# Kernel tuning notes

Hardware: AMD Instinct MI355X
Metric: run time of the kernel (lower is better)

## Reference

```python
import jax, jax.numpy as jnp
import numpy as np

B, S, H, NH = 2, 2048, 768, 12
HD = H // NH
MEM_W = 0.5  # memory_weight
LN_EPS = 1e-5


def setup_inputs() -> dict:
    key = jax.random.key(0)
    ks = jax.random.split(key, 12)
    xav = lambda k: jax.random.uniform(k, (H, H), jnp.float32, -1.0, 1.0) * np.sqrt(6.0 / (H + H))
    return {
        "hidden_states": jax.random.normal(ks[0], (B, S, H), jnp.float32),
        "cross_states": jax.random.normal(ks[1], (B, S, H), jnp.float32),
        "attention_mask": jnp.ones((B, 1, S, S), jnp.int32),
        "memory_tensors": jax.random.normal(ks[2], (2, B, S, H), jnp.float32),
        "dynamic_factor": jax.random.uniform(ks[3], (B, S, 1), jnp.float32),
        "Wq": xav(ks[4]), "bq": jnp.zeros((H,), jnp.float32),
        "Wk": xav(ks[5]), "bk": jnp.zeros((H,), jnp.float32),
        "Wv": xav(ks[6]), "bv": jnp.zeros((H,), jnp.float32),
        "Wo": xav(ks[7]), "bo": jnp.zeros((H,), jnp.float32),
        "gate": jnp.ones((1,), jnp.float32),
        "gate_bias": jnp.zeros((1,), jnp.float32),
        "ln_g": jnp.ones((H,), jnp.float32),
        "ln_b": jnp.zeros((H,), jnp.float32),
    }


def _layernorm(x, g, b):
    mu = jnp.mean(x, axis=-1, keepdims=True)
    var = jnp.mean(jnp.square(x - mu), axis=-1, keepdims=True)
    return (x - mu) * jax.lax.rsqrt(var + LN_EPS) * g + b


def reference(hidden_states, cross_states, attention_mask, memory_tensors,
              dynamic_factor, Wq, bq, Wk, bk, Wv, bv, Wo, bo,
              gate, gate_bias, ln_g, ln_b):
    x = _layernorm(hidden_states, ln_g, ln_b)
    q = x @ Wq + bq                      # [B,S,H]
    k = cross_states @ Wk + bk
    v = cross_states @ Wv + bv
    k = k + memory_tensors[0] * MEM_W    # memory injection into K/V
    v = v + memory_tensors[1] * MEM_W

    q = q.reshape(B, S, NH, HD).transpose(0, 2, 1, 3)  # [B,NH,S,HD]
    k = k.reshape(B, S, NH, HD).transpose(0, 2, 1, 3)
    v = v.reshape(B, S, NH, HD).transpose(0, 2, 1, 3)

    scores = jnp.einsum("bhqd,bhkd->bhqk", q, k) / np.sqrt(HD)
    scores = jnp.where(attention_mask == 0, -jnp.inf, scores)
    attn = jax.nn.softmax(scores, axis=-1)
    out = jnp.einsum("bhqk,bhkd->bhqd", attn, v)       # [B,NH,S,HD]
    out = out.transpose(0, 2, 1, 3).reshape(B, S, H)

    out = out @ Wo + bo
    out = out * gate + gate_bias
    out = out * dynamic_factor
    return out
```

## Files before the change

### kernel.cpp

```cpp
#include <hip/hip_runtime.h>
#include <hip/hip_bf16.h>
#include <stdint.h>

#define BB   2
#define SS   2048
#define HH   768
#define NHH  12
#define HDD  64
#define BSS  (BB*SS)
#define NBH  (BB*NHH)
#define ROWS_BH (NBH*SS)
#define NSPLIT 2

typedef unsigned short u16;
typedef unsigned int   u32;
typedef __attribute__((ext_vector_type(8))) short bf16x8_t;
typedef __attribute__((ext_vector_type(4))) float f32x4;
typedef __attribute__((ext_vector_type(2))) u32   u32x2;
typedef __attribute__((ext_vector_type(4))) u32   u32x4;

#define MFMA16(a, b, c) __builtin_amdgcn_mfma_f32_16x16x32_bf16((a), (b), (c), 0, 0, 0)

__device__ __forceinline__ float b2f(u16 u) {
    u32 x = ((u32)u) << 16; float f; __builtin_memcpy(&f, &x, 4); return f;
}
__device__ __forceinline__ u16 f2b(float f) {
    u32 x; __builtin_memcpy(&x, &f, 4);
    u32 r = x + 0x7fffu + ((x >> 16) & 1u);
    return (u16)(r >> 16);
}
__device__ __forceinline__ void async16(const u16* g, u16* l) {
    __builtin_amdgcn_global_load_lds(
        (const __attribute__((address_space(1))) void*)g,
        (__attribute__((address_space(3))) void*)l, 16, 0, 0);
}

__global__ __launch_bounds__(256) void prep_kernel(
    const float* __restrict__ Wq, const float* __restrict__ Wk,
    const float* __restrict__ Wv, const float* __restrict__ Wo,
    u16* __restrict__ Wt,
    const float* __restrict__ hid, const float* __restrict__ cross,
    const float* __restrict__ g, const float* __restrict__ bb,
    u16* __restrict__ xln, u16* __restrict__ crossb,
    const int* __restrict__ mask, u32* __restrict__ bits,
    u32* __restrict__ wrow)
{
    int id = blockIdx.x;
    int t = threadIdx.x;

    if (id < 576) {
        int mat = id / 144, rem = id % 144;
        int by = rem / 12, bx = rem % 12;
        const float* src = (mat == 0) ? Wq : (mat == 1) ? Wk : (mat == 2) ? Wv : Wo;
        u16* dst = Wt + (size_t)mat * 768 * 768;

        __shared__ float sm[64][68];
        int r0 = by * 64, c0 = bx * 64;
        #pragma unroll
        for (int it = 0; it < 4; ++it) {
            int c = t + it * 256;
            int r = c >> 4, sg = c & 15;
            *(float4*)&sm[r][sg * 4] = *(const float4*)&src[(size_t)(r0 + r) * 768 + c0 + sg * 4];
        }
        __syncthreads();
        #pragma unroll
        for (int it = 0; it < 2; ++it) {
            int c = t + it * 256;
            int rr = c >> 3, sg = c & 7;
            u16 tmp[8] __attribute__((aligned(16)));
            #pragma unroll
            for (int j = 0; j < 8; ++j) tmp[j] = f2b(sm[sg * 8 + j][rr]);
            *(u32x4*)&dst[(size_t)(c0 + rr) * 768 + r0 + sg * 8] = *(u32x4*)tmp;
        }
        return;
    }

    if (id < 2624) {
        int lid = id - 576;
        int y = lid >> 10, bx = lid & 1023;
        int wv = t >> 6, lane = t & 63;
        int row = bx * 4 + wv;

        if (y == 1) {
            const float* xr = cross + (size_t)row * 768;
            u16* o = crossb + (size_t)row * 768;
            #pragma unroll
            for (int c = 0; c < 3; ++c) {
                float4 f = *(const float4*)&xr[c * 256 + lane * 4];
                u16 t4[4] __attribute__((aligned(8)));
                t4[0] = f2b(f.x); t4[1] = f2b(f.y); t4[2] = f2b(f.z); t4[3] = f2b(f.w);
                *(u32x2*)&o[c * 256 + lane * 4] = *(u32x2*)t4;
            }
            return;
        }

        const float* xr = hid + (size_t)row * 768;
        float v[12];
        float s = 0.f, s2 = 0.f;
        #pragma unroll
        for (int c = 0; c < 3; ++c) {
            float4 f = *(const float4*)&xr[c * 256 + lane * 4];
            v[c*4+0] = f.x; v[c*4+1] = f.y; v[c*4+2] = f.z; v[c*4+3] = f.w;
            s  += f.x + f.y + f.z + f.w;
            s2 += f.x*f.x + f.y*f.y + f.z*f.z + f.w*f.w;
        }
        #pragma unroll
        for (int off = 1; off < 64; off <<= 1) {
            s  += __shfl_xor(s,  off, 64);
            s2 += __shfl_xor(s2, off, 64);
        }
        float mu  = s  * (1.f / 768.f);
        float var = s2 * (1.f / 768.f) - mu * mu;
        float rs  = 1.f / sqrtf(var + 1e-5f);
        #pragma unroll
        for (int c = 0; c < 3; ++c) {
            float4 gg = *(const float4*)&g [c * 256 + lane * 4];
            float4 bv = *(const float4*)&bb[c * 256 + lane * 4];
            u16 o[4] __attribute__((aligned(8)));
            o[0] = f2b((v[c*4+0] - mu) * rs * gg.x + bv.x);
            o[1] = f2b((v[c*4+1] - mu) * rs * gg.y + bv.y);
            o[2] = f2b((v[c*4+2] - mu) * rs * gg.z + bv.z);
            o[3] = f2b((v[c*4+3] - mu) * rs * gg.w + bv.w);
            *(u32x2*)&xln[(size_t)row * 768 + c * 256 + lane * 4] = *(u32x2*)o;
        }
        return;
    }

    {
        int mid = id - 2624;
        int w = mid * 256 + t;
        const int4* p = (const int4*)(mask + (size_t)w * 32);
        u32 v = 0;
        #pragma unroll
        for (int i = 0; i < 8; ++i) {
            int4 m = p[i];
            v |= ((m.x != 0) ? 1u : 0u) << (4 * i + 0);
            v |= ((m.y != 0) ? 1u : 0u) << (4 * i + 1);
            v |= ((m.z != 0) ? 1u : 0u) << (4 * i + 2);
            v |= ((m.w != 0) ? 1u : 0u) << (4 * i + 3);
        }
        bits[w] = v;
        unsigned long long ball = __ballot(v == 0xffffffffu);
        if ((t & 63) == 0) {
            u32 wr = 0;
            #pragma unroll
            for (int kt = 0; kt < 32; ++kt)
                if (((ball >> (2 * kt)) & 3ull) == 3ull) wr |= (1u << kt);
            wrow[w >> 6] = wr;
        }
    }
}

__device__ __forceinline__ void gemm128_main(const u16* __restrict__ A,
                                             const u16* __restrict__ W,
                                             f32x4 acc[4][4])
{
    __shared__ __attribute__((aligned(16))) u16 AsL[128 * 64];
    __shared__ __attribute__((aligned(16))) u16 BsL[128 * 64];
    int m0 = blockIdx.x * 128, n0 = blockIdx.y * 128;
    int t = threadIdx.x;
    int wv = t >> 6, lane = t & 63, lm = lane & 15, quad = lane >> 4;
    int wr = wv >> 1, wc = wv & 1;

    for (int kt = 0; kt < 768 / 64; ++kt) {
        __syncthreads();
        #pragma unroll
        for (int it = 0; it < 4; ++it) {
            int c = t + it * 256;
            int row = c >> 3, cs = (c & 7) ^ (row & 7);
            async16(A + (size_t)(m0 + row) * 768 + kt * 64 + cs * 8, &AsL[c * 8]);
            async16(W + (size_t)(n0 + row) * 768 + kt * 64 + cs * 8, &BsL[c * 8]);
        }
        __syncthreads();
        #pragma unroll
        for (int kk = 0; kk < 2; ++kk) {
            bf16x8_t af[4], bfv[4];
            #pragma unroll
            for (int i = 0; i < 4; ++i) {
                int r = wr * 64 + i * 16 + lm;
                af[i] = *(const bf16x8_t*)&AsL[(r * 8 + ((kk * 4 + quad) ^ (r & 7))) * 8];
            }
            #pragma unroll
            for (int j = 0; j < 4; ++j) {
                int r = wc * 64 + j * 16 + lm;
                bfv[j] = *(const bf16x8_t*)&BsL[(r * 8 + ((kk * 4 + quad) ^ (r & 7))) * 8];
            }
            #pragma unroll
            for (int i = 0; i < 4; ++i)
                #pragma unroll
                for (int j = 0; j < 4; ++j)
                    acc[i][j] = MFMA16(af[i], bfv[j], acc[i][j]);
        }
    }
}

__global__ __launch_bounds__(256) void qkv_gemm(
    const u16* __restrict__ xln, const u16* __restrict__ crossb,
    const u16* __restrict__ Wt,  const float* __restrict__ bq,
    const float* __restrict__ bk, const float* __restrict__ bv,
    const float* __restrict__ mem,
    u16* __restrict__ Qb, u16* __restrict__ Kb, u16* __restrict__ VtG)
{
    int z = blockIdx.z;
    const u16* A      = (z == 0) ? xln : crossb;
    const u16* W      = Wt + (size_t)z * 768 * 768;
    const float* bias = (z == 0) ? bq : (z == 1) ? bk : bv;
    const float* mp   = (z == 0) ? (const float*)nullptr : mem + (size_t)(z - 1) * BSS * HH;

    f32x4 z4 = {0.f, 0.f, 0.f, 0.f};
    f32x4 acc[4][4];
    #pragma unroll
    for (int i = 0; i < 4; ++i)
        #pragma unroll
        for (int j = 0; j < 4; ++j) acc[i][j] = z4;

    gemm128_main(A, W, acc);

    int t = threadIdx.x, wv = t >> 6, lane = t & 63, lm = lane & 15, quad = lane >> 4;
    int wr = wv >> 1, wc = wv & 1;
    int row0 = blockIdx.x * 128 + wr * 64 + quad * 4;
    int col0 = blockIdx.y * 128 + wc * 64 + lm;

    if (z == 2) {
        #pragma unroll
        for (int j = 0; j < 4; ++j) {
            int cg = col0 + j * 16;
            float bz = bias[cg];
            int h = cg >> 6, d = cg & 63;
            #pragma unroll
            for (int i = 0; i < 4; ++i) {
                int rg = row0 + i * 16;
                int b = rg >> 11, s = rg & 2047;
                u16 ob[4] __attribute__((aligned(8)));
                #pragma unroll
                for (int e = 0; e < 4; ++e) {
                    float v = acc[i][j][e] + bz + 0.5f * mp[(size_t)(rg + e) * HH + cg];
                    ob[e] = f2b(v);
                }
                *(u32x2*)&VtG[((size_t)(b * NHH + h) * 64 + d) * SS + s] = *(u32x2*)ob;
            }
        }
        return;
    }

    u16* out = (z == 0) ? Qb : Kb;
    #pragma unroll
    for (int j = 0; j < 4; ++j) {
        int cg = col0 + j * 16;
        float bz = bias[cg];
        #pragma unroll
        for (int i = 0; i < 4; ++i) {
            int rg = row0 + i * 16;
            #pragma unroll
            for (int e = 0; e < 4; ++e) {
                float v = acc[i][j][e] + bz;
                if (mp) v += 0.5f * mp[(size_t)(rg + e) * HH + cg];
                out[(size_t)(rg + e) * HH + cg] = f2b(v);
            }
        }
    }
}

__global__ __launch_bounds__(512) void attn_kernel(
    const u16* __restrict__ Q, const u16* __restrict__ K,
    const u16* __restrict__ VtG, const u32* __restrict__ mbits,
    const u32* __restrict__ wrow,
    u16* __restrict__ Pacc, float* __restrict__ Pl, int ksteps)
{
    __shared__ __attribute__((aligned(16))) u16   KsL[64 * 64];
    __shared__ __attribute__((aligned(16))) u16   VtL[64 * 64];
    __shared__ __attribute__((aligned(16))) short Ps[8][16][72];

    int qt = blockIdx.x;
    int bh = blockIdx.y;
    int z  = blockIdx.z;
    int b = bh / NHH, h = bh % NHH;
    int t = threadIdx.x;
    int wv = t >> 6, lane = t & 63, lm = lane & 15, quad = lane >> 4;
    int r7 = lm & 7;

    int qrow_g = b * SS + qt * 128 + wv * 16;
    const u16* qp = Q + (size_t)(qrow_g + lm) * HH + h * 64;
    bf16x8_t qf0 = *(const bf16x8_t*)&qp[quad * 8];
    bf16x8_t qf1 = *(const bf16x8_t*)&qp[32 + quad * 8];

    f32x4 z4 = {0.f, 0.f, 0.f, 0.f};
    f32x4 acc_o[4] = {z4, z4, z4, z4};
    float l_part[4] = {0.f, 0.f, 0.f, 0.f};

    const float SC = 0.18033688011112042f;
    int qloc = qt * 128 + wv * 16 + quad * 4;

    u32 wand = wrow[b * SS + qloc + 0] & wrow[b * SS + qloc + 1] &
               wrow[b * SS + qloc + 2] & wrow[b * SS + qloc + 3];

    int kr = t >> 3, cs = (t & 7) ^ (kr & 7);
    const u16* Kb0 = K + (size_t)(b * SS) * HH + h * 64;
    const u16* Vb0 = VtG + (size_t)bh * 64 * SS;

    int kt0 = z * ksteps;
    for (int kt = kt0; kt < kt0 + ksteps; ++kt) {
        __syncthreads();
        int k0 = kt * 64;
        async16(Kb0 + (size_t)(k0 + kr) * HH + cs * 8, &KsL[t * 8]);
        async16(Vb0 + (size_t)kr * SS + k0 + cs * 8,   &VtL[t * 8]);
        __syncthreads();

        f32x4 sc[4];
        #pragma unroll
        for (int k16 = 0; k16 < 4; ++k16) {
            int rowk = k16 * 16 + lm;
            bf16x8_t kf0 = *(const bf16x8_t*)&KsL[(rowk * 8 + (quad ^ r7)) * 8];
            bf16x8_t kf1 = *(const bf16x8_t*)&KsL[(rowk * 8 + ((quad ^ 4) ^ r7)) * 8];
            f32x4 a = z4;
            a = MFMA16(qf0, kf0, a);
            a = MFMA16(qf1, kf1, a);
            sc[k16] = a;
        }

        if (!__all((int)((wand >> kt) & 1u))) {
            #pragma unroll
            for (int e = 0; e < 4; ++e) {
                u32x2 u = *(const u32x2*)&mbits[(size_t)(b * SS + qloc + e) * (SS / 32) + kt * 2];
                unsigned long long mw = ((unsigned long long)u.y << 32) | (unsigned long long)u.x;
                #pragma unroll
                for (int k16 = 0; k16 < 4; ++k16)
                    if (!((mw >> (k16 * 16 + lm)) & 1ull)) sc[k16][e] = -3.0e38f;
            }
        }

        #pragma unroll
        for (int k16 = 0; k16 < 4; ++k16) {
            #pragma unroll
            for (int e = 0; e < 4; ++e) {
                float p = __builtin_amdgcn_exp2f(sc[k16][e] * SC);
                sc[k16][e] = p;
                l_part[e] += p;
            }
        }

        #pragma unroll
        for (int k16 = 0; k16 < 4; ++k16) {
            int colg = ((k16 + quad) & 3) * 16;
            #pragma unroll
            for (int e = 0; e < 4; ++e) {
                float pv = sc[k16][e];
                u32 pb = __builtin_bit_cast(u32, pv);
                Ps[wv][quad * 4 + e][colg + lm] = (short)((pb + 0x8000u) >> 16);
            }
        }
        __asm__ volatile("" ::: "memory");

        #pragma unroll
        for (int cc = 0; cc < 2; ++cc) {
            int k16r = cc * 2 + (quad >> 1);
            int colg = ((k16r + (lm >> 2)) & 3) * 16 + (quad & 1) * 8;
            bf16x8_t pf = *(const bf16x8_t*)&Ps[wv][lm][colg];
            #pragma unroll
            for (int j = 0; j < 4; ++j) {
                bf16x8_t vf = *(const bf16x8_t*)&VtL[((j * 16 + lm) * 8 + ((cc * 4 + quad) ^ r7)) * 8];
                acc_o[j] = MFMA16(pf, vf, acc_o[j]);
            }
        }
    }

    #pragma unroll
    for (int off = 1; off < 16; off <<= 1) {
        #pragma unroll
        for (int e = 0; e < 4; ++e)
            l_part[e] += __shfl_xor(l_part[e], off, 64);
    }

    size_t prow = ((size_t)z * NBH + bh) * SS + qt * 128 + wv * 16 + quad * 4;
    #pragma unroll
    for (int j = 0; j < 4; ++j)
        #pragma unroll
        for (int e = 0; e < 4; ++e)
            Pacc[(prow + e) * 64 + j * 16 + lm] = f2b(acc_o[j][e]);
    if (lm == 0) {
        #pragma unroll
        for (int e = 0; e < 4; ++e)
            Pl[prow + e] = l_part[e];
    }
}

__global__ __launch_bounds__(256) void attn_merge(
    const u16* __restrict__ Pacc, const float* __restrict__ Pl,
    u16* __restrict__ AO)
{
    int t = threadIdx.x;
    int r = blockIdx.x * 64 + (t >> 2);
    int dseg = (t & 3) * 16;

    float lsum = Pl[r] + Pl[(size_t)ROWS_BH + r];

    float o[16];
    #pragma unroll
    for (int i = 0; i < 16; ++i) o[i] = 0.f;
    #pragma unroll
    for (int s = 0; s < NSPLIT; ++s) {
        const u16* ap = &Pacc[((size_t)s * ROWS_BH + r) * 64 + dseg];
        u32x4 a0 = *(const u32x4*)ap;
        u32x4 a1 = *(const u32x4*)(ap + 8);
        u32 wa[8];
        wa[0]=a0.x; wa[1]=a0.y; wa[2]=a0.z; wa[3]=a0.w;
        wa[4]=a1.x; wa[5]=a1.y; wa[6]=a1.z; wa[7]=a1.w;
        #pragma unroll
        for (int i = 0; i < 8; ++i) {
            o[2*i]   += b2f((u16)(wa[i] & 0xffff));
            o[2*i+1] += b2f((u16)(wa[i] >> 16));
        }
    }
    float inv = 1.f / lsum;
    int bh = r >> 11, q = r & 2047;
    int b = bh / NHH, h = bh % NHH;
    u16 ob[16] __attribute__((aligned(16)));
    #pragma unroll
    for (int i = 0; i < 16; ++i) ob[i] = f2b(o[i] * inv);
    u16* op = &AO[((size_t)(b * SS + q)) * HH + h * 64 + dseg];
    *(u32x4*)op       = *(u32x4*)ob;
    *(u32x4*)(op + 8) = *(u32x4*)(ob + 8);
}

__global__ __launch_bounds__(256) void out_gemm(
    const u16* __restrict__ AO, const u16* __restrict__ Wt,
    const float* __restrict__ bo, const float* __restrict__ gate,
    const float* __restrict__ gbias, const float* __restrict__ dyn,
    float* __restrict__ out)
{
    f32x4 z4 = {0.f, 0.f, 0.f, 0.f};
    f32x4 acc[4][4];
    #pragma unroll
    for (int i = 0; i < 4; ++i)
        #pragma unroll
        for (int j = 0; j < 4; ++j) acc[i][j] = z4;

    gemm128_main(AO, Wt, acc);

    float gv = gate[0];
    float gb = gbias[0];
    int t = threadIdx.x, wv = t >> 6, lane = t & 63, lm = lane & 15, quad = lane >> 4;
    int wr = wv >> 1, wc = wv & 1;
    int row0 = blockIdx.x * 128 + wr * 64 + quad * 4;
    int col0 = blockIdx.y * 128 + wc * 64 + lm;
    #pragma unroll
    for (int j = 0; j < 4; ++j) {
        int cg = col0 + j * 16;
        float bz = bo[cg];
        #pragma unroll
        for (int i = 0; i < 4; ++i) {
            int rg = row0 + i * 16;
            #pragma unroll
            for (int e = 0; e < 4; ++e) {
                float v = acc[i][j][e] + bz;
                v = v * gv + gb;
                v *= dyn[rg + e];
                out[(size_t)(rg + e) * HH + cg] = v;
            }
        }
    }
}

extern "C" void kernel_launch(void* const* d_in, const int* in_sizes, int n_in,
                              void* d_out, int out_size, void* d_ws, size_t ws_size,
                              hipStream_t stream)
{
    (void)in_sizes; (void)n_in; (void)out_size; (void)ws_size;

    const float* hid   = (const float*)d_in[0];
    const float* cross = (const float*)d_in[1];
    const int*   amask = (const int*)d_in[2];
    const float* mem   = (const float*)d_in[3];
    const float* dyn   = (const float*)d_in[4];
    const float* Wq    = (const float*)d_in[5];
    const float* bq    = (const float*)d_in[6];
    const float* Wk    = (const float*)d_in[7];
    const float* bk    = (const float*)d_in[8];
    const float* Wv    = (const float*)d_in[9];
    const float* bv    = (const float*)d_in[10];
    const float* Wo    = (const float*)d_in[11];
    const float* bo    = (const float*)d_in[12];
    const float* gate  = (const float*)d_in[13];
    const float* gbias = (const float*)d_in[14];
    const float* lng   = (const float*)d_in[15];
    const float* lnb   = (const float*)d_in[16];

    char* p = (char*)d_ws;
    u16* Wt   = (u16*)p; p += (size_t)4 * 768 * 768 * 2;
    u32* mb   = (u32*)p; p += (size_t)BB * SS * (SS / 32) * 4;
    u32* wrow = (u32*)p; p += (size_t)BSS * 4;
    u16* xln  = (u16*)p; p += (size_t)BSS * HH * 2;
    u16* crb  = (u16*)p; p += (size_t)BSS * HH * 2;
    u16* Qb   = (u16*)p; p += (size_t)BSS * HH * 2;
    u16* Kb   = (u16*)p; p += (size_t)BSS * HH * 2;
    u16* VtG  = (u16*)p; p += (size_t)BSS * HH * 2;
    u16* Pacc  = xln;
    float* Pl  = (float*)Wt;
    u16* AO    = Kb;

    prep_kernel <<<dim3(3648),           256, 0, stream>>>(
        Wq, Wk, Wv, Wo, Wt, hid, cross, lng, lnb, xln, crb, amask, mb, wrow);
    qkv_gemm    <<<dim3(32, 6, 3),       256, 0, stream>>>(
        xln, crb, Wt, bq, bk, bv, mem, Qb, Kb, VtG);
    attn_kernel <<<dim3(16, 24, NSPLIT), 512, 0, stream>>>(
        Qb, Kb, VtG, mb, wrow, Pacc, Pl, SS / 64 / NSPLIT);
    attn_merge  <<<dim3(ROWS_BH / 64),   256, 0, stream>>>(Pacc, Pl, AO);
    out_gemm    <<<dim3(32, 6),          256, 0, stream>>>(
        AO, Wt + (size_t)3 * 768 * 768, bo, gate, gbias, dyn, (float*)d_out);
}
```

Measured before the change: 262.2 us.

## Double-buffer LDS tiles in GEMMs and attention, move GEMMs to 8 waves

The attention kernel and the shared GEMM mainloop now use double-buffered LDS tiles. The next K/V or A/W tile is prefetched asynchronously while the current one is consumed, and only one barrier is needed per iteration. This is meant to hide global-load latency behind MFMA work. The GEMMs also move from 256 to 512 threads with a 4x2 MFMA tile per wave and a K-step of 32, and they drop the XOR swizzle on the LDS layout. Dropping the swizzle risks LDS bank conflicts, and the smaller per-wave tile gives less reuse per fragment load.

Measured after the change: 266.4 us. About the same (+1.6%).

```diff
diff --git a/kernel.cpp b/kernel.cpp
--- a/kernel.cpp
+++ b/kernel.cpp
@@ -153,48 +153,44 @@
 
 __device__ __forceinline__ void gemm128_main(const u16* __restrict__ A,
                                              const u16* __restrict__ W,
-                                             f32x4 acc[4][4])
-{
-    __shared__ __attribute__((aligned(16))) u16 AsL[128 * 64];
-    __shared__ __attribute__((aligned(16))) u16 BsL[128 * 64];
+                                             f32x4 acc[4][2])
+{
+    __shared__ __attribute__((aligned(16))) u16 AsL[2][128 * 32];
+    __shared__ __attribute__((aligned(16))) u16 BsL[2][128 * 32];
     int m0 = blockIdx.x * 128, n0 = blockIdx.y * 128;
     int t = threadIdx.x;
     int wv = t >> 6, lane = t & 63, lm = lane & 15, quad = lane >> 4;
-    int wr = wv >> 1, wc = wv & 1;
-
-    for (int kt = 0; kt < 768 / 64; ++kt) {
+    int wr = wv >> 2, wc = wv & 3;
+
+    const u16* Ap = A + (size_t)(m0 + (t >> 2)) * 768 + (t & 3) * 8;
+    const u16* Bp = W + (size_t)(n0 + (t >> 2)) * 768 + (t & 3) * 8;
+
+    async16(Ap, &AsL[0][t * 8]);
+    async16(Bp, &BsL[0][t * 8]);
+
+    for (int kt = 0; kt < 768 / 32; ++kt) {
+        int cur = kt & 1;
         __syncthreads();
-        #pragma unroll
-        for (int it = 0; it < 4; ++it) {
-            int c = t + it * 256;
-            int row = c >> 3, cs = (c & 7) ^ (row & 7);
-            async16(A + (size_t)(m0 + row) * 768 + kt * 64 + cs * 8, &AsL[c * 8]);
-            async16(W + (size_t)(n0 + row) * 768 + kt * 64 + cs * 8, &BsL[c * 8]);
-        }
-        __syncthreads();
-        #pragma unroll
-        for (int kk = 0; kk < 2; ++kk) {
-            bf16x8_t af[4], bfv[4];
-            #pragma unroll
-            for (int i = 0; i < 4; ++i) {
-                int r = wr * 64 + i * 16 + lm;
-                af[i] = *(const bf16x8_t*)&AsL[(r * 8 + ((kk * 4 + quad) ^ (r & 7))) * 8];
-            }
-            #pragma unroll
-            for (int j = 0; j < 4; ++j) {
-                int r = wc * 64 + j * 16 + lm;
-                bfv[j] = *(const bf16x8_t*)&BsL[(r * 8 + ((kk * 4 + quad) ^ (r & 7))) * 8];
-            }
-            #pragma unroll
-            for (int i = 0; i < 4; ++i)
-                #pragma unroll
-                for (int j = 0; j < 4; ++j)
-                    acc[i][j] = MFMA16(af[i], bfv[j], acc[i][j]);
-        }
-    }
-}
-
-__global__ __launch_bounds__(256) void qkv_gemm(
+        if (kt + 1 < 768 / 32) {
+            async16(Ap + (kt + 1) * 32, &AsL[cur ^ 1][t * 8]);
+            async16(Bp + (kt + 1) * 32, &BsL[cur ^ 1][t * 8]);
+        }
+        bf16x8_t af[4], bfv[2];
+        #pragma unroll
+        for (int i = 0; i < 4; ++i)
+            af[i]  = *(const bf16x8_t*)&AsL[cur][(wr * 64 + i * 16 + lm) * 32 + quad * 8];
+        #pragma unroll
+        for (int j = 0; j < 2; ++j)
+            bfv[j] = *(const bf16x8_t*)&BsL[cur][(wc * 32 + j * 16 + lm) * 32 + quad * 8];
+        #pragma unroll
+        for (int i = 0; i < 4; ++i)
+            #pragma unroll
+            for (int j = 0; j < 2; ++j)
+                acc[i][j] = MFMA16(af[i], bfv[j], acc[i][j]);
+    }
+}
+
+__global__ __launch_bounds__(512) void qkv_gemm(
     const u16* __restrict__ xln, const u16* __restrict__ crossb,
     const u16* __restrict__ Wt,  const float* __restrict__ bq,
     const float* __restrict__ bk, const float* __restrict__ bv,
@@ -208,22 +204,22 @@
     const float* mp   = (z == 0) ? (const float*)nullptr : mem + (size_t)(z - 1) * BSS * HH;
 
     f32x4 z4 = {0.f, 0.f, 0.f, 0.f};
-    f32x4 acc[4][4];
+    f32x4 acc[4][2];
     #pragma unroll
     for (int i = 0; i < 4; ++i)
         #pragma unroll
-        for (int j = 0; j < 4; ++j) acc[i][j] = z4;
+        for (int j = 0; j < 2; ++j) acc[i][j] = z4;
 
     gemm128_main(A, W, acc);
 
     int t = threadIdx.x, wv = t >> 6, lane = t & 63, lm = lane & 15, quad = lane >> 4;
-    int wr = wv >> 1, wc = wv & 1;
+    int wr = wv >> 2, wc = wv & 3;
     int row0 = blockIdx.x * 128 + wr * 64 + quad * 4;
-    int col0 = blockIdx.y * 128 + wc * 64 + lm;
+    int col0 = blockIdx.y * 128 + wc * 32 + lm;
 
     if (z == 2) {
         #pragma unroll
-        for (int j = 0; j < 4; ++j) {
+        for (int j = 0; j < 2; ++j) {
             int cg = col0 + j * 16;
             float bz = bias[cg];
             int h = cg >> 6, d = cg & 63;
@@ -245,7 +241,7 @@
 
     u16* out = (z == 0) ? Qb : Kb;
     #pragma unroll
-    for (int j = 0; j < 4; ++j) {
+    for (int j = 0; j < 2; ++j) {
         int cg = col0 + j * 16;
         float bz = bias[cg];
         #pragma unroll
@@ -267,8 +263,8 @@
     const u32* __restrict__ wrow,
     u16* __restrict__ Pacc, float* __restrict__ Pl, int ksteps)
 {
-    __shared__ __attribute__((aligned(16))) u16   KsL[64 * 64];
-    __shared__ __attribute__((aligned(16))) u16   VtL[64 * 64];
+    __shared__ __attribute__((aligned(16))) u16   KsL[2][64 * 64];
+    __shared__ __attribute__((aligned(16))) u16   VtL[2][64 * 64];
     __shared__ __attribute__((aligned(16))) short Ps[8][16][72];
 
     int qt = blockIdx.x;
@@ -299,19 +295,24 @@
     const u16* Vb0 = VtG + (size_t)bh * 64 * SS;
 
     int kt0 = z * ksteps;
+    async16(Kb0 + (size_t)(kt0 * 64 + kr) * HH + cs * 8, &KsL[0][t * 8]);
+    async16(Vb0 + (size_t)kr * SS + kt0 * 64 + cs * 8,   &VtL[0][t * 8]);
+
     for (int kt = kt0; kt < kt0 + ksteps; ++kt) {
+        int cur = (kt - kt0) & 1;
         __syncthreads();
-        int k0 = kt * 64;
-        async16(Kb0 + (size_t)(k0 + kr) * HH + cs * 8, &KsL[t * 8]);
-        async16(Vb0 + (size_t)kr * SS + k0 + cs * 8,   &VtL[t * 8]);
-        __syncthreads();
+        if (kt + 1 < kt0 + ksteps) {
+            int kn = (kt + 1) * 64;
+            async16(Kb0 + (size_t)(kn + kr) * HH + cs * 8, &KsL[cur ^ 1][t * 8]);
+            async16(Vb0 + (size_t)kr * SS + kn + cs * 8,   &VtL[cur ^ 1][t * 8]);
+        }
 
         f32x4 sc[4];
         #pragma unroll
         for (int k16 = 0; k16 < 4; ++k16) {
             int rowk = k16 * 16 + lm;
-            bf16x8_t kf0 = *(const bf16x8_t*)&KsL[(rowk * 8 + (quad ^ r7)) * 8];
-            bf16x8_t kf1 = *(const bf16x8_t*)&KsL[(rowk * 8 + ((quad ^ 4) ^ r7)) * 8];
+            bf16x8_t kf0 = *(const bf16x8_t*)&KsL[cur][(rowk * 8 + (quad ^ r7)) * 8];
+            bf16x8_t kf1 = *(const bf16x8_t*)&KsL[cur][(rowk * 8 + ((quad ^ 4) ^ r7)) * 8];
             f32x4 a = z4;
             a = MFMA16(qf0, kf0, a);
             a = MFMA16(qf1, kf1, a);
@@ -358,7 +359,7 @@
             bf16x8_t pf = *(const bf16x8_t*)&Ps[wv][lm][colg];
             #pragma unroll
             for (int j = 0; j < 4; ++j) {
-                bf16x8_t vf = *(const bf16x8_t*)&VtL[((j * 16 + lm) * 8 + ((cc * 4 + quad) ^ r7)) * 8];
+                bf16x8_t vf = *(const bf16x8_t*)&VtL[cur][((j * 16 + lm) * 8 + ((cc * 4 + quad) ^ r7)) * 8];
                 acc_o[j] = MFMA16(pf, vf, acc_o[j]);
             }
         }
@@ -422,29 +423,29 @@
     *(u32x4*)(op + 8) = *(u32x4*)(ob + 8);
 }
 
-__global__ __launch_bounds__(256) void out_gemm(
+__global__ __launch_bounds__(512) void out_gemm(
     const u16* __restrict__ AO, const u16* __restrict__ Wt,
     const float* __restrict__ bo, const float* __restrict__ gate,
     const float* __restrict__ gbias, const float* __restrict__ dyn,
     float* __restrict__ out)
 {
     f32x4 z4 = {0.f, 0.f, 0.f, 0.f};
-    f32x4 acc[4][4];
+    f32x4 acc[4][2];
     #pragma unroll
     for (int i = 0; i < 4; ++i)
         #pragma unroll
-        for (int j = 0; j < 4; ++j) acc[i][j] = z4;
+        for (int j = 0; j < 2; ++j) acc[i][j] = z4;
 
     gemm128_main(AO, Wt, acc);
 
     float gv = gate[0];
     float gb = gbias[0];
     int t = threadIdx.x, wv = t >> 6, lane = t & 63, lm = lane & 15, quad = lane >> 4;
-    int wr = wv >> 1, wc = wv & 1;
+    int wr = wv >> 2, wc = wv & 3;
     int row0 = blockIdx.x * 128 + wr * 64 + quad * 4;
-    int col0 = blockIdx.y * 128 + wc * 64 + lm;
-    #pragma unroll
-    for (int j = 0; j < 4; ++j) {
+    int col0 = blockIdx.y * 128 + wc * 32 + lm;
+    #pragma unroll
+    for (int j = 0; j < 2; ++j) {
         int cg = col0 + j * 16;
         float bz = bo[cg];
         #pragma unroll
@@ -500,11 +501,11 @@
 
     prep_kernel <<<dim3(3648),           256, 0, stream>>>(
         Wq, Wk, Wv, Wo, Wt, hid, cross, lng, lnb, xln, crb, amask, mb, wrow);
-    qkv_gemm    <<<dim3(32, 6, 3),       256, 0, stream>>>(
+    qkv_gemm    <<<dim3(32, 6, 3),       512, 0, stream>>>(
         xln, crb, Wt, bq, bk, bv, mem, Qb, Kb, VtG);
     attn_kernel <<<dim3(16, 24, NSPLIT), 512, 0, stream>>>(
         Qb, Kb, VtG, mb, wrow, Pacc, Pl, SS / 64 / NSPLIT);
     attn_merge  <<<dim3(ROWS_BH / 64),   256, 0, stream>>>(Pacc, Pl, AO);
-    out_gemm    <<<dim3(32, 6),          256, 0, stream>>>(
+    out_gemm    <<<dim3(32, 6),          512, 0, stream>>>(
         AO, Wt + (size_t)3 * 768 * 768, bo, gate, gbias, dyn, (float*)d_out);
 }
```
